# Kernel tuning notes

Measured on AMD Instinct MI355X. Metric: run time of the kernel, lower is better.

The kernel has to match this reference:

```python
import jax, jax.numpy as jnp
import numpy as np

HIDDEN = 64
CLUSTERS = 25
NUM_CLASSES = 10
N_NODES = 9600
N_FEAT = 128
B_GRAPHS = 64
NODES_PER_GRAPH = N_NODES // B_GRAPHS


def setup_inputs() -> dict:
    key = jax.random.key(0)
    ks = jax.random.split(key, 16)
    # node features
    x = jax.random.normal(ks[0], (N_NODES, N_FEAT), dtype=jnp.float32)
    # block-diagonal symmetric adjacency (p=0.05 within each graph block)
    seg_ids = jnp.repeat(jnp.arange(B_GRAPHS, dtype=jnp.int32), NODES_PER_GRAPH)
    block_mask = (seg_ids[:, None] == seg_ids[None, :]).astype(jnp.float32)
    r = jax.random.uniform(ks[1], (N_NODES, N_NODES), dtype=jnp.float32)
    a = (r < 0.05).astype(jnp.float32) * block_mask
    a = jnp.maximum(a, a.T)  # symmetrize
    a = a * (1.0 - jnp.eye(N_NODES, dtype=jnp.float32))  # no explicit self loops (GCN adds them)

    def glorot(k, shape):
        lim = np.sqrt(6.0 / (shape[0] + shape[1]))
        return jax.random.uniform(k, shape, dtype=jnp.float32, minval=-lim, maxval=lim)

    params = dict(
        W1=glorot(ks[2], (N_FEAT, HIDDEN)), b1=jnp.zeros((HIDDEN,), jnp.float32),
        W2=glorot(ks[3], (HIDDEN, HIDDEN)), b2=jnp.zeros((HIDDEN,), jnp.float32),
        Wa=glorot(ks[4], (HIDDEN, CLUSTERS)), ba=jnp.zeros((CLUSTERS,), jnp.float32),
        Wp=glorot(ks[5], (HIDDEN, HIDDEN)), bp=jnp.zeros((HIDDEN,), jnp.float32),
        Wc=glorot(ks[6], (HIDDEN, NUM_CLASSES)), bc=jnp.zeros((NUM_CLASSES,), jnp.float32),
    )
    return dict(x=x, a=a, seg_ids=seg_ids, num_graphs=B_GRAPHS, **params)


def _gcn(a, x, W, b):
    n = a.shape[0]
    ah = a + jnp.eye(n, dtype=a.dtype)
    d_isqrt = jax.lax.rsqrt(jnp.maximum(ah.sum(axis=1), 1e-12))
    an = d_isqrt[:, None] * ah * d_isqrt[None, :]
    return an @ (x @ W) + b


def reference(x, a, seg_ids, num_graphs, W1, b1, W2, b2, Wa, ba, Wp, bp, Wc, bc):
    B = int(num_graphs)
    C = CLUSTERS
    N = x.shape[0]
    # --- encode: two GCN layers (dropout = identity at inference) ---
    Z = jax.nn.relu(_gcn(a, x, W1, b1))
    Z = jax.nn.relu(_gcn(a, Z, W2, b2))  # [N, H]
    # --- batched DiffPool ---
    # assignment via GCN, softmax over per-graph clusters
    S = jax.nn.softmax(_gcn(a, Z, Wa, ba), axis=-1)  # [N, C]
    # place each node's assignment row into its graph's cluster block -> block-diagonal S_big [N, B*C]
    cols = seg_ids[:, None].astype(jnp.int32) * C + jnp.arange(C, dtype=jnp.int32)[None, :]
    S_big = jnp.zeros((N, B * C), dtype=S.dtype).at[jnp.arange(N)[:, None], cols].set(S)
    Zp = S_big.T @ Z                 # [B*C, H]
    Ap = S_big.T @ (a @ S_big)       # [B*C, B*C], block diagonal
    # --- post GCN on pooled graph + relu ---
    H = jax.nn.relu(_gcn(Ap, Zp, Wp, bp))  # [B*C, H]
    # --- global sum pool readout over pooled nodes per graph ---
    seg_p = jnp.repeat(jnp.arange(B, dtype=jnp.int32), C)
    G_emb = jax.ops.segment_sum(H, seg_p, num_segments=B)  # [B, H]
    logits = G_emb @ Wc + bc  # [B, num_classes]
    return logits
```

## Files before the change

### kernel.cpp

```cpp
#include <hip/hip_runtime.h>

#define NG   64
#define NPG  150
#define NN   9600
#define NF   128
#define NH   64
#define NC   25
#define NCLS 10
#define ELLW 40

typedef unsigned short u16;
typedef unsigned long long u64;

__global__ __launch_bounds__(256) void k_prep(const float* __restrict__ a,
                                              float* __restrict__ dsi,
                                              int* __restrict__ cnt,
                                              u16* __restrict__ ell) {
  int n = (blockIdx.x * 256 + threadIdx.x) >> 6;
  int lane = threadIdx.x & 63;
  if (n >= NN) return;
  int g0 = (n / NPG) * NPG;
  int i = n - g0;
  const float* arow = a + (size_t)n * NN + g0;
  float v0 = arow[lane];
  float v1 = arow[64 + lane];
  float v2 = 0.f;
  if (lane < NPG - 128) v2 = arow[128 + lane];
  u64 m0 = __ballot(v0 != 0.f && lane != i);
  u64 m1 = __ballot(v1 != 0.f && (64 + lane) != i);
  u64 m2 = __ballot(lane < NPG - 128 && v2 != 0.f && (128 + lane) != i);
  int p0 = __popcll(m0), p1 = __popcll(m1), p2 = __popcll(m2);
  u16* er = ell + (size_t)n * ELLW;
  u64 below = (lane == 0) ? 0ull : (~0ull >> (64 - lane));
  if ((m0 >> lane) & 1) { int s = 1 + __popcll(m0 & below);           if (s < ELLW) er[s] = (u16)lane; }
  if ((m1 >> lane) & 1) { int s = 1 + p0 + __popcll(m1 & below);      if (s < ELLW) er[s] = (u16)(64 + lane); }
  if ((m2 >> lane) & 1) { int s = 1 + p0 + p1 + __popcll(m2 & below); if (s < ELLW) er[s] = (u16)(128 + lane); }
  if (lane == 0) {
    er[0] = (u16)i;
    int deg = 1 + p0 + p1 + p2;
    cnt[n] = (deg < ELLW) ? deg : ELLW;
    dsi[n] = rsqrtf((float)deg);
  }
}

template <int K>
__global__ __launch_bounds__(256) void k_mmW(const float* __restrict__ A,
                                             const float* __restrict__ W,
                                             float* __restrict__ C) {
  __shared__ float sW[K * NH];
  int t = threadIdx.x;
  for (int m = t; m < K * NH; m += 256) sW[m] = W[m];
  __syncthreads();
  int h = t & 63, rg = t >> 6;
  int r0 = blockIdx.x * 16 + rg * 4;
  const float* a0 = A + (size_t)r0 * K;
  float c0 = 0.f, c1 = 0.f, c2 = 0.f, c3 = 0.f;
  for (int k = 0; k < K; ++k) {
    float w = sW[k * NH + h];
    c0 = fmaf(a0[k],         w, c0);
    c1 = fmaf(a0[K + k],     w, c1);
    c2 = fmaf(a0[2 * K + k], w, c2);
    c3 = fmaf(a0[3 * K + k], w, c3);
  }
  float* cp = C + (size_t)r0 * NH + h;
  cp[0] = c0; cp[NH] = c1; cp[2 * NH] = c2; cp[3 * NH] = c3;
}

__global__ __launch_bounds__(256) void k_prop(const float* __restrict__ T,
                                              const float* __restrict__ dsi,
                                              const int* __restrict__ cnt,
                                              const u16* __restrict__ ell,
                                              const float* __restrict__ b,
                                              float* __restrict__ Z) {
  int n = (blockIdx.x * 256 + threadIdx.x) >> 6;
  int h = threadIdx.x & 63;
  if (n >= NN) return;
  int g0 = (n / NPG) * NPG;
  const u16* er = ell + (size_t)n * ELLW;
  int cn = cnt[n];
  const float* Tg = T + (size_t)g0 * NH;
  const float* dg = dsi + g0;
  float a0 = 0.f, a1 = 0.f;
  int e = 0;
  for (; e + 1 < cn; e += 2) {
    int ja = er[e], jb = er[e + 1];
    a0 = fmaf(dg[ja], Tg[ja * NH + h], a0);
    a1 = fmaf(dg[jb], Tg[jb * NH + h], a1);
  }
  if (e < cn) { int ja = er[e]; a0 = fmaf(dg[ja], Tg[ja * NH + h], a0); }
  Z[(size_t)n * NH + h] = fmaxf(fmaf(dsi[n], a0 + a1, b[h]), 0.f);
}

__global__ __launch_bounds__(256) void k_prop2t3(const float* __restrict__ T,
                                                 const float* __restrict__ dsi,
                                                 const int* __restrict__ cnt,
                                                 const u16* __restrict__ ell,
                                                 const float* __restrict__ b,
                                                 const float* __restrict__ Wa,
                                                 float* __restrict__ Z,
                                                 float* __restrict__ T3) {
  __shared__ float sZ[4][NH];
  int n = (blockIdx.x * 256 + threadIdx.x) >> 6;
  int h = threadIdx.x & 63;
  int w = (threadIdx.x >> 6) & 3;
  if (n >= NN) return;
  int g0 = (n / NPG) * NPG;
  const u16* er = ell + (size_t)n * ELLW;
  int cn = cnt[n];
  const float* Tg = T + (size_t)g0 * NH;
  const float* dg = dsi + g0;
  float a0 = 0.f, a1 = 0.f;
  int e = 0;
  for (; e + 1 < cn; e += 2) {
    int ja = er[e], jb = er[e + 1];
    a0 = fmaf(dg[ja], Tg[ja * NH + h], a0);
    a1 = fmaf(dg[jb], Tg[jb * NH + h], a1);
  }
  if (e < cn) { int ja = er[e]; a0 = fmaf(dg[ja], Tg[ja * NH + h], a0); }
  float z = fmaxf(fmaf(dsi[n], a0 + a1, b[h]), 0.f);
  Z[(size_t)n * NH + h] = z;
  sZ[w][h] = z;
  if (h < NC) {
    const float* zr = sZ[w];
    float t0 = 0.f, t1 = 0.f;
    for (int k = 0; k < NH; k += 2) {
      t0 = fmaf(zr[k],     Wa[k * NC + h],       t0);
      t1 = fmaf(zr[k + 1], Wa[(k + 1) * NC + h], t1);
    }
    T3[(size_t)n * 26 + h] = t0 + t1;
  }
}

__global__ __launch_bounds__(512, 1) void k_tail(
    const float* __restrict__ Z2, const float* __restrict__ T3g,
    const float* __restrict__ dsiG, const int* __restrict__ cntG,
    const u16* __restrict__ ellG,
    const float* __restrict__ ba, const float* __restrict__ Wp,
    const float* __restrict__ bp, const float* __restrict__ Wc,
    const float* __restrict__ bc, float* __restrict__ out) {
  __shared__ float sT3[NPG * 26];
  __shared__ float sS[NPG * 26];
  __shared__ float sdsi[NPG];
  __shared__ int   scnt[NPG];
  __shared__ float sZp[NC * NH];
  __shared__ float sAp[NC * 26];
  __shared__ float sdsiP[NC];
  __shared__ float sU[NC * NH];
  __shared__ float sHp[NC * NH];
  __shared__ float sG[NH];

  const int g = blockIdx.x, t = threadIdx.x;
  const int base = g * NPG;
  const float* Z2g = Z2 + (size_t)base * NH;
  const u16* ellg = ellG + (size_t)base * ELLW;

  if (t < NPG) { sdsi[t] = dsiG[base + t]; scnt[t] = cntG[base + t]; }
  for (int idx = t; idx < NPG * 26; idx += 512)
    sT3[idx] = T3g[(size_t)base * 26 + idx];
  __syncthreads();

  for (int idx = t; idx < NPG * 26; idx += 512) {
    int i = idx / 26, c = idx - i * 26;
    if (c < NC) {
      int cn = scnt[i];
      const u16* er = ellg + i * ELLW;
      float a0 = 0.f;
      for (int e = 0; e < cn; ++e) { int j = er[e]; a0 = fmaf(sdsi[j], sT3[j * 26 + c], a0); }
      sS[idx] = fmaf(sdsi[i], a0, ba[c]);
    }
  }
  __syncthreads();

  if (t < NPG) {
    float* r = sS + t * 26;
    float mx = r[0];
    for (int c = 1; c < NC; ++c) mx = fmaxf(mx, r[c]);
    float s = 0.f;
    for (int c = 0; c < NC; ++c) { float e = expf(r[c] - mx); r[c] = e; s += e; }
    float inv = 1.f / s;
    for (int c = 0; c < NC; ++c) r[c] *= inv;
  }
  __syncthreads();

  for (int idx = t; idx < NPG * 26; idx += 512) {
    int i = idx / 26, c = idx - i * 26;
    if (c < NC) {
      int cn = scnt[i];
      const u16* er = ellg + i * ELLW;
      float a0 = 0.f;
      for (int e = 1; e < cn; ++e) a0 += sS[er[e] * 26 + c];
      sT3[idx] = a0;
    }
  }
  __syncthreads();

  for (int idx = t; idx < NC * NH; idx += 512) {
    int r = idx >> 6, h = idx & 63;
    float a0 = 0.f, a1 = 0.f;
    for (int i = 0; i < NPG; i += 2) {
      a0 = fmaf(sS[i * 26 + r],       Z2g[i * NH + h],       a0);
      a1 = fmaf(sS[(i + 1) * 26 + r], Z2g[(i + 1) * NH + h], a1);
    }
    sZp[idx] = a0 + a1;
  }
  for (int idx = t; idx < NC * NC; idx += 512) {
    int r = idx / NC, c = idx - r * NC;
    float a0 = 0.f, a1 = 0.f;
    for (int i = 0; i < NPG; i += 2) {
      a0 = fmaf(sS[i * 26 + r],       sT3[i * 26 + c],       a0);
      a1 = fmaf(sS[(i + 1) * 26 + r], sT3[(i + 1) * 26 + c], a1);
    }
    sAp[r * 26 + c] = a0 + a1;
  }
  __syncthreads();

  if (t < NC) {
    float d = 1.f;
    for (int c = 0; c < NC; ++c) d += sAp[t * 26 + c];
    sdsiP[t] = rsqrtf(d);
  }
  __syncthreads();

  for (int idx = t; idx < NC * NH; idx += 512) {
    int r = idx >> 6, h = idx & 63;
    float a0 = 0.f;
    for (int k = 0; k < NH; ++k) a0 = fmaf(sZp[r * NH + k], Wp[k * NH + h], a0);
    sU[idx] = sdsiP[r] * a0;
  }
  __syncthreads();

  for (int idx = t; idx < NC * NH; idx += 512) {
    int r = idx >> 6, h = idx & 63;
    float a0 = sU[idx];
    for (int c = 0; c < NC; ++c) a0 = fmaf(sAp[r * 26 + c], sU[c * NH + h], a0);
    sHp[idx] = fmaxf(fmaf(sdsiP[r], a0, bp[h]), 0.f);
  }
  __syncthreads();

  if (t < NH) {
    float s = 0.f;
    for (int r = 0; r < NC; ++r) s += sHp[r * NH + t];
    sG[t] = s;
  }
  __syncthreads();

  if (t < NCLS) {
    float acc = bc[t];
    for (int h = 0; h < NH; ++h) acc = fmaf(sG[h], Wc[h * NCLS + t], acc);
    out[g * NCLS + t] = acc;
  }
}

extern "C" void kernel_launch(void* const* d_in, const int* in_sizes, int n_in,
                              void* d_out, int out_size, void* d_ws, size_t ws_size,
                              hipStream_t stream) {
  (void)in_sizes; (void)n_in; (void)out_size; (void)ws_size;
  const float* x  = (const float*)d_in[0];
  const float* a  = (const float*)d_in[1];
  const float* W1 = (const float*)d_in[4];
  const float* b1 = (const float*)d_in[5];
  const float* W2 = (const float*)d_in[6];
  const float* b2 = (const float*)d_in[7];
  const float* Wa = (const float*)d_in[8];
  const float* ba = (const float*)d_in[9];
  const float* Wp = (const float*)d_in[10];
  const float* bp = (const float*)d_in[11];
  const float* Wc = (const float*)d_in[12];
  const float* bc = (const float*)d_in[13];
  float* out = (float*)d_out;

  char* ws = (char*)d_ws;
  float* dsi = (float*)(ws + 0);
  int*   cnt = (int*)  (ws + 38400);
  u16*   ell = (u16*)  (ws + 76800);
  float* T1  = (float*)(ws + 844800);
  float* Z1  = (float*)(ws + 3302400);
  float* T2  = (float*)(ws + 5760000);
  float* Z2  = (float*)(ws + 8217600);
  float* T3  = (float*)(ws + 10675200);

  k_prep    <<<2400, 256, 0, stream>>>(a, dsi, cnt, ell);
  k_mmW<NF> <<<600,  256, 0, stream>>>(x, W1, T1);
  k_prop    <<<2400, 256, 0, stream>>>(T1, dsi, cnt, ell, b1, Z1);
  k_mmW<NH> <<<600,  256, 0, stream>>>(Z1, W2, T2);
  k_prop2t3 <<<2400, 256, 0, stream>>>(T2, dsi, cnt, ell, b2, Wa, Z2, T3);
  k_tail    <<<NG,   512, 0, stream>>>(Z2, T3, dsi, cnt, ell, ba, Wp, bp, Wc, bc, out);
}
```

Measured before the change: 516.5 us.

## Merge prep with first matmul and fuse layer-1 propagation with W2 multiply

The adjacency-scan prep kernel and the x@W1 matmul now run in one launch, with blocks split by index between the two independent tasks. The layer-1 propagation now stages each node's ReLU output in shared memory and immediately multiplies by W2, so the Z1 intermediate and a separate matmul kernel are gone. This removes two launches and a global round trip of Z1. The cost is that the combined kernel reserves 32KB of shared memory for every block, including the prep blocks that never use it, which can lower occupancy; W2 is also read from global memory per thread rather than from a shared tile.

Result: no change. 512.5 us (-0.8%).

```diff
diff --git a/kernel.cpp b/kernel.cpp
--- a/kernel.cpp
+++ b/kernel.cpp
@@ -12,68 +12,71 @@
 typedef unsigned short u16;
 typedef unsigned long long u64;
 
-__global__ __launch_bounds__(256) void k_prep(const float* __restrict__ a,
-                                              float* __restrict__ dsi,
-                                              int* __restrict__ cnt,
-                                              u16* __restrict__ ell) {
-  int n = (blockIdx.x * 256 + threadIdx.x) >> 6;
-  int lane = threadIdx.x & 63;
-  if (n >= NN) return;
-  int g0 = (n / NPG) * NPG;
-  int i = n - g0;
-  const float* arow = a + (size_t)n * NN + g0;
-  float v0 = arow[lane];
-  float v1 = arow[64 + lane];
-  float v2 = 0.f;
-  if (lane < NPG - 128) v2 = arow[128 + lane];
-  u64 m0 = __ballot(v0 != 0.f && lane != i);
-  u64 m1 = __ballot(v1 != 0.f && (64 + lane) != i);
-  u64 m2 = __ballot(lane < NPG - 128 && v2 != 0.f && (128 + lane) != i);
-  int p0 = __popcll(m0), p1 = __popcll(m1), p2 = __popcll(m2);
-  u16* er = ell + (size_t)n * ELLW;
-  u64 below = (lane == 0) ? 0ull : (~0ull >> (64 - lane));
-  if ((m0 >> lane) & 1) { int s = 1 + __popcll(m0 & below);           if (s < ELLW) er[s] = (u16)lane; }
-  if ((m1 >> lane) & 1) { int s = 1 + p0 + __popcll(m1 & below);      if (s < ELLW) er[s] = (u16)(64 + lane); }
-  if ((m2 >> lane) & 1) { int s = 1 + p0 + p1 + __popcll(m2 & below); if (s < ELLW) er[s] = (u16)(128 + lane); }
-  if (lane == 0) {
-    er[0] = (u16)i;
-    int deg = 1 + p0 + p1 + p2;
-    cnt[n] = (deg < ELLW) ? deg : ELLW;
-    dsi[n] = rsqrtf((float)deg);
-  }
-}
-
-template <int K>
-__global__ __launch_bounds__(256) void k_mmW(const float* __restrict__ A,
-                                             const float* __restrict__ W,
-                                             float* __restrict__ C) {
-  __shared__ float sW[K * NH];
-  int t = threadIdx.x;
-  for (int m = t; m < K * NH; m += 256) sW[m] = W[m];
-  __syncthreads();
-  int h = t & 63, rg = t >> 6;
-  int r0 = blockIdx.x * 16 + rg * 4;
-  const float* a0 = A + (size_t)r0 * K;
-  float c0 = 0.f, c1 = 0.f, c2 = 0.f, c3 = 0.f;
-  for (int k = 0; k < K; ++k) {
-    float w = sW[k * NH + h];
-    c0 = fmaf(a0[k],         w, c0);
-    c1 = fmaf(a0[K + k],     w, c1);
-    c2 = fmaf(a0[2 * K + k], w, c2);
-    c3 = fmaf(a0[3 * K + k], w, c3);
-  }
-  float* cp = C + (size_t)r0 * NH + h;
-  cp[0] = c0; cp[NH] = c1; cp[2 * NH] = c2; cp[3 * NH] = c3;
-}
-
-__global__ __launch_bounds__(256) void k_prop(const float* __restrict__ T,
-                                              const float* __restrict__ dsi,
-                                              const int* __restrict__ cnt,
-                                              const u16* __restrict__ ell,
-                                              const float* __restrict__ b,
-                                              float* __restrict__ Z) {
+__global__ __launch_bounds__(256) void k_prep_mm1(const float* __restrict__ a,
+                                                  const float* __restrict__ x,
+                                                  const float* __restrict__ W1,
+                                                  float* __restrict__ dsi,
+                                                  int* __restrict__ cnt,
+                                                  u16* __restrict__ ell,
+                                                  float* __restrict__ T1) {
+  __shared__ float sW[NF * NH];
+  if (blockIdx.x < 2400) {
+    int n = (blockIdx.x * 256 + threadIdx.x) >> 6;
+    int lane = threadIdx.x & 63;
+    if (n >= NN) return;
+    int g0 = (n / NPG) * NPG;
+    int i = n - g0;
+    const float* arow = a + (size_t)n * NN + g0;
+    float v0 = arow[lane];
+    float v1 = arow[64 + lane];
+    float v2 = 0.f;
+    if (lane < NPG - 128) v2 = arow[128 + lane];
+    u64 m0 = __ballot(v0 != 0.f && lane != i);
+    u64 m1 = __ballot(v1 != 0.f && (64 + lane) != i);
+    u64 m2 = __ballot(lane < NPG - 128 && v2 != 0.f && (128 + lane) != i);
+    int p0 = __popcll(m0), p1 = __popcll(m1), p2 = __popcll(m2);
+    u16* er = ell + (size_t)n * ELLW;
+    u64 below = (lane == 0) ? 0ull : (~0ull >> (64 - lane));
+    if ((m0 >> lane) & 1) { int s = 1 + __popcll(m0 & below);           if (s < ELLW) er[s] = (u16)lane; }
+    if ((m1 >> lane) & 1) { int s = 1 + p0 + __popcll(m1 & below);      if (s < ELLW) er[s] = (u16)(64 + lane); }
+    if ((m2 >> lane) & 1) { int s = 1 + p0 + p1 + __popcll(m2 & below); if (s < ELLW) er[s] = (u16)(128 + lane); }
+    if (lane == 0) {
+      er[0] = (u16)i;
+      int deg = 1 + p0 + p1 + p2;
+      cnt[n] = (deg < ELLW) ? deg : ELLW;
+      dsi[n] = rsqrtf((float)deg);
+    }
+  } else {
+    int t = threadIdx.x;
+    for (int m = t; m < NF * NH; m += 256) sW[m] = W1[m];
+    __syncthreads();
+    int h = t & 63, rg = t >> 6;
+    int r0 = (blockIdx.x - 2400) * 16 + rg * 4;
+    const float* a0 = x + (size_t)r0 * NF;
+    float c0 = 0.f, c1 = 0.f, c2 = 0.f, c3 = 0.f;
+    for (int k = 0; k < NF; ++k) {
+      float w = sW[k * NH + h];
+      c0 = fmaf(a0[k],          w, c0);
+      c1 = fmaf(a0[NF + k],     w, c1);
+      c2 = fmaf(a0[2 * NF + k], w, c2);
+      c3 = fmaf(a0[3 * NF + k], w, c3);
+    }
+    float* cp = T1 + (size_t)r0 * NH + h;
+    cp[0] = c0; cp[NH] = c1; cp[2 * NH] = c2; cp[3 * NH] = c3;
+  }
+}
+
+__global__ __launch_bounds__(256) void k_prop_mm2(const float* __restrict__ T,
+                                                  const float* __restrict__ dsi,
+                                                  const int* __restrict__ cnt,
+                                                  const u16* __restrict__ ell,
+                                                  const float* __restrict__ b,
+                                                  const float* __restrict__ W2,
+                                                  float* __restrict__ T2) {
+  __shared__ float sZ[4][NH];
   int n = (blockIdx.x * 256 + threadIdx.x) >> 6;
   int h = threadIdx.x & 63;
+  int w = (threadIdx.x >> 6) & 3;
   if (n >= NN) return;
   int g0 = (n / NPG) * NPG;
   const u16* er = ell + (size_t)n * ELLW;
@@ -88,7 +91,14 @@
     a1 = fmaf(dg[jb], Tg[jb * NH + h], a1);
   }
   if (e < cn) { int ja = er[e]; a0 = fmaf(dg[ja], Tg[ja * NH + h], a0); }
-  Z[(size_t)n * NH + h] = fmaxf(fmaf(dsi[n], a0 + a1, b[h]), 0.f);
+  sZ[w][h] = fmaxf(fmaf(dsi[n], a0 + a1, b[h]), 0.f);
+  const float* zr = sZ[w];
+  float t0 = 0.f, t1 = 0.f;
+  for (int k = 0; k < NH; k += 2) {
+    t0 = fmaf(zr[k],     W2[k * NH + h],       t0);
+    t1 = fmaf(zr[k + 1], W2[(k + 1) * NH + h], t1);
+  }
+  T2[(size_t)n * NH + h] = t0 + t1;
 }
 
 __global__ __launch_bounds__(256) void k_prop2t3(const float* __restrict__ T,
@@ -274,15 +284,12 @@
   int*   cnt = (int*)  (ws + 38400);
   u16*   ell = (u16*)  (ws + 76800);
   float* T1  = (float*)(ws + 844800);
-  float* Z1  = (float*)(ws + 3302400);
-  float* T2  = (float*)(ws + 5760000);
-  float* Z2  = (float*)(ws + 8217600);
-  float* T3  = (float*)(ws + 10675200);
-
-  k_prep    <<<2400, 256, 0, stream>>>(a, dsi, cnt, ell);
-  k_mmW<NF> <<<600,  256, 0, stream>>>(x, W1, T1);
-  k_prop    <<<2400, 256, 0, stream>>>(T1, dsi, cnt, ell, b1, Z1);
-  k_mmW<NH> <<<600,  256, 0, stream>>>(Z1, W2, T2);
+  float* T2  = (float*)(ws + 3302400);
+  float* Z2  = (float*)(ws + 5760000);
+  float* T3  = (float*)(ws + 8217600);
+
+  k_prep_mm1<<<3000, 256, 0, stream>>>(a, x, W1, dsi, cnt, ell, T1);
+  k_prop_mm2<<<2400, 256, 0, stream>>>(T1, dsi, cnt, ell, b1, W2, T2);
   k_prop2t3 <<<2400, 256, 0, stream>>>(T2, dsi, cnt, ell, b2, Wa, Z2, T3);
   k_tail    <<<NG,   512, 0, stream>>>(Z2, T3, dsi, cnt, ell, ba, Wp, bp, Wc, bc, out);
 }
```
